# Optimization experiments

Hardware: AMD Instinct MI355X
Metric: run time of the kernel (lower is better)

## Reference

```python
import jax, jax.numpy as jnp
import numpy as np

V, E, H, O = 50000, 256, 256, 2
B, T = 64, 512


def setup_inputs() -> dict:
    key = jax.random.key(0)
    ks = jax.random.split(key, 16)
    s = 0.05
    return {
        "x": jax.random.randint(ks[0], (B, T), 0, V, dtype=jnp.int64),
        "emb": jax.random.normal(ks[1], (V, E), jnp.float32) * s,
        "w_ih_f": jax.random.normal(ks[2], (4 * H, E), jnp.float32) * s,
        "w_hh_f": jax.random.normal(ks[3], (4 * H, H), jnp.float32) * s,
        "b_ih_f": jax.random.normal(ks[4], (4 * H,), jnp.float32) * s,
        "b_hh_f": jax.random.normal(ks[5], (4 * H,), jnp.float32) * s,
        "w_ih_b": jax.random.normal(ks[6], (4 * H, E), jnp.float32) * s,
        "w_hh_b": jax.random.normal(ks[7], (4 * H, H), jnp.float32) * s,
        "b_ih_b": jax.random.normal(ks[8], (4 * H,), jnp.float32) * s,
        "b_hh_b": jax.random.normal(ks[9], (4 * H,), jnp.float32) * s,
        "fc1_w": jax.random.normal(ks[10], (24, 2 * H), jnp.float32) * s,
        "fc1_b": jax.random.normal(ks[11], (24,), jnp.float32) * s,
        "fc2_w": jax.random.normal(ks[12], (O, 24), jnp.float32) * s,
        "fc2_b": jax.random.normal(ks[13], (O,), jnp.float32) * s,
    }


def _run_lstm(xs, Wih, Whh, b):
    # xs: [T, B, E]; PyTorch gate order i, f, g, o
    Bn = xs.shape[1]
    Hn = Whh.shape[1]
    xproj = jnp.einsum('tbe,ge->tbg', xs, Wih) + b  # precompute input projections

    def step(carry, xt):
        h, c = carry
        z = xt + h @ Whh.T
        i, f, g, o = jnp.split(z, 4, axis=-1)
        c = jax.nn.sigmoid(f) * c + jax.nn.sigmoid(i) * jnp.tanh(g)
        h = jax.nn.sigmoid(o) * jnp.tanh(c)
        return (h, c), h

    h0 = jnp.zeros((Bn, Hn), xs.dtype)
    _, ys = jax.lax.scan(step, (h0, h0), xproj)
    return ys  # [T, B, H]


def reference(x, emb, w_ih_f, w_hh_f, b_ih_f, b_hh_f,
              w_ih_b, w_hh_b, b_ih_b, b_hh_b,
              fc1_w, fc1_b, fc2_w, fc2_b):
    embedded = emb[x]                       # [B, T, E]
    xs = jnp.transpose(embedded, (1, 0, 2))  # [T, B, E]
    ys_f = _run_lstm(xs, w_ih_f, w_hh_f, b_ih_f + b_hh_f)          # forward dir
    ys_b = _run_lstm(xs[::-1], w_ih_b, w_hh_b, b_ih_b + b_hh_b)    # backward dir
    # output[:, -1, :] = concat(fwd hidden at t=T-1, bwd hidden at t=T-1)
    # bwd hidden at original t=T-1 is the first step of the reversed scan.
    lstm_out = jnp.concatenate([ys_f[-1], ys_b[0]], axis=-1)  # [B, 2H]
    fc1_out = jax.nn.relu(lstm_out @ fc1_w.T + fc1_b)
    return fc1_out @ fc2_w.T + fc2_b
```

## Files before the change

kernel.cpp:

```cpp
#include <hip/hip_runtime.h>

typedef unsigned int  u32;
typedef unsigned short u16;
typedef unsigned long long u64;
typedef _Float16 half8 __attribute__((ext_vector_type(8)));
typedef short   short8 __attribute__((ext_vector_type(8)));
typedef float   f32x4  __attribute__((ext_vector_type(4)));

#define T_LEN 512
#define BATCH 64
#define EDIM  256
#define HDIM  256
#define G4    1024

static __device__ __forceinline__ u16 f2bf(float f) {
  u32 u = __builtin_bit_cast(u32, f);
  u = (u + 0x7fffu + ((u >> 16) & 1u)) >> 16;
  return (u16)u;
}
static __device__ __forceinline__ u16 f2h(float a) {
  _Float16 ha = (_Float16)a;
  return __builtin_bit_cast(u16, ha);
}
static __device__ __forceinline__ float h2f(u16 a) {
  return (float)__builtin_bit_cast(_Float16, a);
}
static __device__ __forceinline__ float sigf(float x) {
  return __builtin_amdgcn_rcpf(1.0f + __expf(-x));
}
static __device__ __forceinline__ float tanhfast(float x) {
  return fmaf(2.0f, __builtin_amdgcn_rcpf(1.0f + __expf(-2.0f * x)), -1.0f);
}

__global__ __launch_bounds__(256) void k_prep(const float* __restrict__ whh,
                                              u16* __restrict__ Wf,
                                              u16* __restrict__ Wst) {
  int cell = blockIdx.x * 256 + threadIdx.x;
  int mt = cell >> 9, kt = (cell >> 6) & 7, l = cell & 63;
  int gr = mt * 16 + (l & 15);
  int c0 = kt * 32 + (l >> 4) * 8;
  const float4* src = (const float4*)(whh + (size_t)gr * 256 + c0);
  float4 a = src[0], b = src[1];
  u16 o[8] = { f2h(a.x), f2h(a.y), f2h(a.z), f2h(a.w),
               f2h(b.x), f2h(b.y), f2h(b.z), f2h(b.w) };
  *(uint4*)(Wf + (size_t)cell * 8) = *(uint4*)o;
  if (kt >= 6) {
    int q = mt >> 4, jj = mt & 15, s = (kt - 6) * 4 + q;
    *(uint4*)(Wst + ((size_t)(jj * 8 + s) * 64 + l) * 8) = *(uint4*)o;
  }
}

#define LDSPITCH 264
__global__ __launch_bounds__(256) void k_xproj(const int* __restrict__ x,
                                               const float* __restrict__ emb,
                                               const float* __restrict__ wih,
                                               const float* __restrict__ bih,
                                               const float* __restrict__ bhh,
                                               u16* __restrict__ xp2) {
  __shared__ u16 smA[64 * LDSPITCH];
  __shared__ u16 smB[64 * LDSPITCH];
  const int tn = blockIdx.x, t = blockIdx.y;
  const int tid = threadIdx.x;
  const int r = tid >> 2, q4 = tid & 3;

  {
    int eidx = x[r * T_LEN + t];
    const float4* src = (const float4*)(emb + (size_t)eidx * EDIM + q4 * 64);
    u16* dst = smA + r * LDSPITCH + q4 * 64;
    #pragma unroll
    for (int i = 0; i < 16; ++i) {
      float4 v = src[i];
      uint2 p;
      p.x = (u32)f2bf(v.x) | ((u32)f2bf(v.y) << 16);
      p.y = (u32)f2bf(v.z) | ((u32)f2bf(v.w) << 16);
      *(uint2*)&dst[i * 4] = p;
    }
  }
  {
    const float4* src = (const float4*)(wih + (size_t)(tn * 64 + r) * EDIM + q4 * 64);
    u16* dst = smB + r * LDSPITCH + q4 * 64;
    #pragma unroll
    for (int i = 0; i < 16; ++i) {
      float4 v = src[i];
      uint2 p;
      p.x = (u32)f2bf(v.x) | ((u32)f2bf(v.y) << 16);
      p.y = (u32)f2bf(v.z) | ((u32)f2bf(v.w) << 16);
      *(uint2*)&dst[i * 4] = p;
    }
  }
  __syncthreads();

  const int wv = tid >> 6, lane = tid & 63;
  const int lm = lane & 15, q = lane >> 4;
  f32x4 acc[4];
  #pragma unroll
  for (int nt = 0; nt < 4; ++nt) acc[nt] = (f32x4){0.f, 0.f, 0.f, 0.f};

  const u16* pa = smA + (wv * 16 + lm) * LDSPITCH + q * 8;
  const u16* pb = smB + lm * LDSPITCH + q * 8;
  #pragma unroll
  for (int ks = 0; ks < 8; ++ks) {
    short8 av = *(const short8*)(pa + ks * 32);
    #pragma unroll
    for (int nt = 0; nt < 4; ++nt) {
      short8 bv = *(const short8*)(pb + nt * 16 * LDSPITCH + ks * 32);
      acc[nt] = __builtin_amdgcn_mfma_f32_16x16x32_bf16(av, bv, acc[nt], 0, 0, 0);
    }
  }
  #pragma unroll
  for (int nt = 0; nt < 4; ++nt) {
    int g = tn * 64 + nt * 16 + lm;
    float bias = bih[g] + bhh[g];
    int gq = g >> 8, j16 = (g >> 4) & 15, qdd = (g & 15) >> 2, rb = g & 3;
    int mtp = j16 * 4 + gq;
    #pragma unroll
    for (int rr = 0; rr < 4; ++rr) {
      int bl = q * 4 + rr;
      size_t idx = ((((size_t)t * 4 + wv) * 64 + mtp) * 64 + (qdd * 16 + bl)) * 4 + rb;
      xp2[idx] = f2h(acc[nt][rr] + bias);
    }
  }
}

__global__ __launch_bounds__(1024, 4) void k_rnn(const u16* __restrict__ Wf,
                                                 const u16* __restrict__ Wst,
                                                 const u16* __restrict__ xp2,
                                                 u16* __restrict__ hf) {
  extern __shared__ u16 sm[];
  u16* smW = sm;
  u16* smH = sm + 65536;
  const int bg = blockIdx.x;
  const int tid = threadIdx.x;
  const int v = tid >> 6, l = tid & 63;
  const int j = v;
  const int bl = l & 15, qd = l >> 4;

  half8 Wr[4][4];
  #pragma unroll
  for (int q = 0; q < 4; ++q)
    #pragma unroll
    for (int kt = 0; kt < 4; ++kt)
      Wr[q][kt] = *(const half8*)(Wf + ((size_t)((q * 16 + j) * 8 + kt) * 64 + l) * 8);
  #pragma unroll
  for (int q = 0; q < 4; ++q)
    asm volatile("" : "+v"(Wr[q][0]), "+v"(Wr[q][1]), "+v"(Wr[q][2]), "+v"(Wr[q][3]));

  #pragma unroll
  for (int q = 0; q < 4; ++q)
    #pragma unroll
    for (int ki = 0; ki < 2; ++ki) {
      uint4 tv = *(const uint4*)(Wf + ((size_t)((q * 16 + j) * 8 + 4 + ki) * 64 + l) * 8);
      *(uint4*)(smW + ((size_t)(v * 8 + q * 2 + ki) * 512 + l * 8)) = tv;
    }

  {
    u32* hz = (u32*)smH;
    for (int i = tid; i < 4224; i += 1024) hz[i] = 0;
  }
  __syncthreads();

  float c[4] = {0.f, 0.f, 0.f, 0.f};

  const u16* xbase = xp2 + (size_t)bg * 16384 + (size_t)j * 1024 + l * 4;
  const u16* hrd0 = smH + bl * 264 + qd * 8;
  const int  hwof = bl * 264 + j * 16 + qd * 4;
  const u16* wst_l = Wst + (size_t)j * 4096 + l * 8;

  uint2 xA[4], xB[4];
  #pragma unroll
  for (int q = 0; q < 4; ++q)
    xA[q] = *(const uint2*)(xbase + q * 256);

#define STEP(T, XC, XN) do {                                                   \
    u32 zoff = 0;                                                              \
    asm volatile("" : "+v"(zoff));      \
    const u16* wp = wst_l + zoff;                                              \
    uint4 S6[4];                                                               \
    _Pragma("unroll")                                                          \
    for (int q = 0; q < 4; ++q)                                                \
      S6[q] = *(const uint4*)(wp + q * 512);                                   \
    _Pragma("unroll")                             \
    for (int q = 0; q < 4; ++q)                                                \
      XN[q] = *(const uint2*)(xbase + 65536 + q * 256);                        \
    const u16* hb = hrd0 + ((T) & 1) * 4224;                                   \
    f32x4 acc[4];                           \
    _Pragma("unroll")                                                          \
    for (int q = 0; q < 4; ++q)                                                \
      acc[q] = (f32x4){ h2f((u16)XC[q].x), h2f((u16)(XC[q].x >> 16)),          \
                        h2f((u16)XC[q].y), h2f((u16)(XC[q].y >> 16)) };        \
    _Pragma("unroll")                                                          \
    for (int kt = 0; kt < 4; ++kt) {                    \
      half8 Bf = *(const half8*)(hb + kt * 32);                                \
      _Pragma("unroll")                                                        \
      for (int q = 0; q < 4; ++q)                                              \
        acc[q] = __builtin_amdgcn_mfma_f32_16x16x32_f16(Wr[q][kt], Bf,         \
                                                        acc[q], 0, 0, 0);      \
    }                                                                          \
    _Pragma("unroll")                                                          \
    for (int kt = 4; kt < 6; ++kt) {                   \
      half8 Bf = *(const half8*)(hb + kt * 32);                                \
      _Pragma("unroll")                                                        \
      for (int q = 0; q < 4; ++q) {                                            \
        half8 Af = *(const half8*)(smW +                                       \
                     ((size_t)(v * 8 + q * 2 + (kt - 4)) * 512 + l * 8));      \
        acc[q] = __builtin_amdgcn_mfma_f32_16x16x32_f16(Af, Bf,                \
                                                        acc[q], 0, 0, 0);      \
      }                                                                        \
    }                                                                          \
    {                                                                          \
      half8 Bf = *(const half8*)(hb + 6 * 32);        \
      _Pragma("unroll")                                                        \
      for (int q = 0; q < 4; ++q)                                              \
        acc[q] = __builtin_amdgcn_mfma_f32_16x16x32_f16(                       \
            __builtin_bit_cast(half8, S6[q]), Bf, acc[q], 0, 0, 0);            \
    }                                                                          \
    uint4 S7[4];                                             \
    _Pragma("unroll")                                                          \
    for (int q = 0; q < 4; ++q)                                                \
      S7[q] = *(const uint4*)(wp + 2048 + q * 512);                            \
    {                                                                          \
      half8 Bf = *(const half8*)(hb + 7 * 32);                    \
      _Pragma("unroll")                                                        \
      for (int q = 0; q < 4; ++q)                                              \
        acc[q] = __builtin_amdgcn_mfma_f32_16x16x32_f16(                       \
            __builtin_bit_cast(half8, S7[q]), Bf, acc[q], 0, 0, 0);            \
    }                                                                          \
    float hn[4];                         \
    _Pragma("unroll")                                                          \
    for (int r = 0; r < 4; ++r) {                                              \
      float zi = acc[0][r], zf = acc[1][r], zg = acc[2][r], zo = acc[3][r];    \
      c[r] = sigf(zf) * c[r] + sigf(zi) * tanhfast(zg);                        \
      hn[r] = sigf(zo) * tanhfast(c[r]);                                       \
    }                                                                          \
    u32 lo = __builtin_bit_cast(u32, __builtin_amdgcn_cvt_pkrtz(hn[0], hn[1]));\
    u32 hi = __builtin_bit_cast(u32, __builtin_amdgcn_cvt_pkrtz(hn[2], hn[3]));\
    if ((T) == T_LEN - 1) {                                                    \
      *(uint2*)(hf + (size_t)(bg * 16 + bl) * 256 + j * 16 + qd * 4) =         \
          make_uint2(lo, hi);                                                  \
    } else {                                                                   \
      *(uint2*)(smH + (((T) + 1) & 1) * 4224 + hwof) = make_uint2(lo, hi);     \
    }                                                                          \
    xbase += 65536;                                                            \
    asm volatile("s_waitcnt lgkmcnt(0)\n\ts_barrier" ::: "memory");            \
  } while (0)

  for (int tt = 0; tt < T_LEN; tt += 2) {
    STEP(tt, xA, xB);
    STEP(tt + 1, xB, xA);
  }
#undef STEP
}

__global__ __launch_bounds__(256) void k_tail(const int* __restrict__ x,
                                              const float* __restrict__ emb,
                                              const float* __restrict__ wihb,
                                              const float* __restrict__ bihb,
                                              const float* __restrict__ bhhb,
                                              const float* __restrict__ fc1w,
                                              const float* __restrict__ fc1b,
                                              const float* __restrict__ fc2w,
                                              const float* __restrict__ fc2b,
                                              const u16* __restrict__ hf,
                                              float* __restrict__ out) {
  const int b = blockIdx.x, tid = threadIdx.x;
  __shared__ float e[EDIM], hb[HDIM], hfl[HDIM], f1[24];
  e[tid]   = emb[(size_t)x[b * T_LEN + (T_LEN - 1)] * EDIM + tid];
  hfl[tid] = h2f(hf[b * HDIM + tid]);
  __syncthreads();

  float z[4];
  #pragma unroll
  for (int gq = 0; gq < 4; ++gq) {
    int g = gq * HDIM + tid;
    float s = bihb[g] + bhhb[g];
    const float4* wr = (const float4*)(wihb + (size_t)g * EDIM);
    #pragma unroll 8
    for (int k = 0; k < 64; ++k) {
      float4 w = wr[k];
      s += w.x * e[4 * k] + w.y * e[4 * k + 1] + w.z * e[4 * k + 2] + w.w * e[4 * k + 3];
    }
    z[gq] = s;
  }
  float cb = sigf(z[0]) * tanhfast(z[2]);
  hb[tid] = sigf(z[3]) * tanhfast(cb);
  __syncthreads();

  if (tid < 24) {
    float s = fc1b[tid];
    const float* w = fc1w + tid * 512;
    #pragma unroll 8
    for (int k = 0; k < HDIM; ++k) s += w[k] * hfl[k] + w[HDIM + k] * hb[k];
    f1[tid] = fmaxf(s, 0.f);
  }
  __syncthreads();
  if (tid < 2) {
    float s = fc2b[tid];
    #pragma unroll
    for (int k = 0; k < 24; ++k) s += fc2w[tid * 24 + k] * f1[k];
    out[b * 2 + tid] = s;
  }
}

extern "C" void kernel_launch(void* const* d_in, const int* in_sizes, int n_in,
                              void* d_out, int out_size, void* d_ws, size_t ws_size,
                              hipStream_t stream) {
  const int*   x     = (const int*)  d_in[0];
  const float* emb   = (const float*)d_in[1];
  const float* wih_f = (const float*)d_in[2];
  const float* whh_f = (const float*)d_in[3];
  const float* bih_f = (const float*)d_in[4];
  const float* bhh_f = (const float*)d_in[5];
  const float* wih_b = (const float*)d_in[6];
  const float* bih_b = (const float*)d_in[8];
  const float* bhh_b = (const float*)d_in[9];
  const float* fc1w  = (const float*)d_in[10];
  const float* fc1b  = (const float*)d_in[11];
  const float* fc2w  = (const float*)d_in[12];
  const float* fc2b  = (const float*)d_in[13];
  float* out = (float*)d_out;

  char* ws = (char*)d_ws;
  u16* xp2  = (u16*)ws;
  u16* Wf   = (u16*)(ws + 67108864);
  u16* Wst  = (u16*)(ws + 67108864 + 524288);
  u16* hf16 = (u16*)(ws + 67108864 + 524288 + 131072);

  k_prep <<<128, 256, 0, stream>>>(whh_f, Wf, Wst);
  k_xproj<<<dim3(16, 512), 256, 0, stream>>>(x, emb, wih_f, bih_f, bhh_f, xp2);
  k_rnn  <<<4, 1024, 147968, stream>>>(Wf, Wst, xp2, hf16);
  k_tail <<<BATCH, 256, 0, stream>>>(x, emb, wih_b, bih_b, bhh_b,
                                     fc1w, fc1b, fc2w, fc2b, hf16, out);
}
```

Before: 1.491 ms.

## Halve RNN block size, give each wave two hidden slices with more register-resident weights

The recurrent kernel now runs 512 threads per block instead of 1024, and each wave handles two 16-wide hidden slices in sequence. More of the W_hh tiles stay in registers (5 of 8 k-tiles instead of 4), while shared memory and global streaming cover the rest. The intent is cheaper per-step barriers with fewer waves and less weight traffic from LDS and global memory. The cost is twice the serial MFMA work per wave on the critical path and much higher register pressure, which risks spills.

```diff
diff --git a/kernel.cpp b/kernel.cpp
--- a/kernel.cpp
+++ b/kernel.cpp
@@ -122,66 +122,82 @@
   }
 }
 
-__global__ __launch_bounds__(1024, 4) void k_rnn(const u16* __restrict__ Wf,
-                                                 const u16* __restrict__ Wst,
-                                                 const u16* __restrict__ xp2,
-                                                 u16* __restrict__ hf) {
+__global__ __launch_bounds__(512, 2) void k_rnn(const u16* __restrict__ Wf,
+                                                const u16* __restrict__ Wst,
+                                                const u16* __restrict__ xp2,
+                                                u16* __restrict__ hf) {
   extern __shared__ u16 sm[];
   u16* smW = sm;
   u16* smH = sm + 65536;
   const int bg = blockIdx.x;
   const int tid = threadIdx.x;
   const int v = tid >> 6, l = tid & 63;
-  const int j = v;
   const int bl = l & 15, qd = l >> 4;
 
-  half8 Wr[4][4];
-  #pragma unroll
-  for (int q = 0; q < 4; ++q)
-    #pragma unroll
-    for (int kt = 0; kt < 4; ++kt)
-      Wr[q][kt] = *(const half8*)(Wf + ((size_t)((q * 16 + j) * 8 + kt) * 64 + l) * 8);
-  #pragma unroll
-  for (int q = 0; q < 4; ++q)
-    asm volatile("" : "+v"(Wr[q][0]), "+v"(Wr[q][1]), "+v"(Wr[q][2]), "+v"(Wr[q][3]));
-
-  #pragma unroll
-  for (int q = 0; q < 4; ++q)
-    #pragma unroll
-    for (int ki = 0; ki < 2; ++ki) {
-      uint4 tv = *(const uint4*)(Wf + ((size_t)((q * 16 + j) * 8 + 4 + ki) * 64 + l) * 8);
-      *(uint4*)(smW + ((size_t)(v * 8 + q * 2 + ki) * 512 + l * 8)) = tv;
-    }
+  half8 Wr[2][4][5];
+  #pragma unroll
+  for (int p = 0; p < 2; ++p) {
+    const int j = 2 * v + p;
+    #pragma unroll
+    for (int q = 0; q < 4; ++q)
+      #pragma unroll
+      for (int kt = 0; kt < 5; ++kt)
+        Wr[p][q][kt] = *(const half8*)(Wf + ((size_t)((q * 16 + j) * 8 + kt) * 64 + l) * 8);
+  }
+  #pragma unroll
+  for (int p = 0; p < 2; ++p)
+    #pragma unroll
+    for (int q = 0; q < 4; ++q)
+      asm volatile("" : "+v"(Wr[p][q][0]), "+v"(Wr[p][q][1]), "+v"(Wr[p][q][2]),
+                        "+v"(Wr[p][q][3]), "+v"(Wr[p][q][4]));
+
+  #pragma unroll
+  for (int p = 0; p < 2; ++p) {
+    const int j = 2 * v + p;
+    #pragma unroll
+    for (int q = 0; q < 4; ++q)
+      #pragma unroll
+      for (int kt = 5; kt < 7; ++kt) {
+        uint4 tv = *(const uint4*)(Wf + ((size_t)((q * 16 + j) * 8 + kt) * 64 + l) * 8);
+        *(uint4*)(smW + (size_t)(v * 16 + (p * 4 + q) * 2 + (kt - 5)) * 512 + l * 8) = tv;
+      }
+  }
 
   {
     u32* hz = (u32*)smH;
-    for (int i = tid; i < 4224; i += 1024) hz[i] = 0;
-  }
-  __syncthreads();
-
-  float c[4] = {0.f, 0.f, 0.f, 0.f};
-
-  const u16* xbase = xp2 + (size_t)bg * 16384 + (size_t)j * 1024 + l * 4;
+    #pragma unroll
+    for (int k = 0; k < 9; ++k) { int i = tid + k * 512; if (i < 4224) hz[i] = 0; }
+  }
+  __syncthreads();
+
+  float c[2][4];
+  #pragma unroll
+  for (int p = 0; p < 2; ++p)
+    #pragma unroll
+    for (int r = 0; r < 4; ++r) c[p][r] = 0.f;
+
+  const u16* xbase = xp2 + (size_t)bg * 16384 + (size_t)l * 4;
   const u16* hrd0 = smH + bl * 264 + qd * 8;
-  const int  hwof = bl * 264 + j * 16 + qd * 4;
-  const u16* wst_l = Wst + (size_t)j * 4096 + l * 8;
+  const int  hwb  = bl * 264 + qd * 4;
+  const u16* wst0 = Wst + (size_t)(2 * v) * 4096 + l * 8;
 
   uint2 xA[4], xB[4];
   #pragma unroll
   for (int q = 0; q < 4; ++q)
-    xA[q] = *(const uint2*)(xbase + q * 256);
-
-#define STEP(T, XC, XN) do {                                                   \
+    xA[q] = *(const uint2*)(xbase + (size_t)(2 * v) * 1024 + q * 256);
+
+#define PASS(P, XC, XN, NXOFF, T) do {                                         \
+    const int j = 2 * v + (P);                                                 \
     u32 zoff = 0;                                                              \
-    asm volatile("" : "+v"(zoff));      \
-    const u16* wp = wst_l + zoff;                                              \
-    uint4 S6[4];                                                               \
+    asm volatile("" : "+v"(zoff));        \
+    const u16* wp = wst0 + (P) * 4096 + zoff;                                  \
+    uint4 S7[4];                                                               \
     _Pragma("unroll")                                                          \
     for (int q = 0; q < 4; ++q)                                                \
-      S6[q] = *(const uint4*)(wp + q * 512);                                   \
+      S7[q] = *(const uint4*)(wp + (4 + q) * 512);                             \
     _Pragma("unroll")                             \
     for (int q = 0; q < 4; ++q)                                                \
-      XN[q] = *(const uint2*)(xbase + 65536 + q * 256);                        \
+      XN[q] = *(const uint2*)(xbase + (NXOFF) + q * 256);                      \
     const u16* hb = hrd0 + ((T) & 1) * 4224;                                   \
     f32x4 acc[4];                           \
     _Pragma("unroll")                                                          \
@@ -189,37 +205,26 @@
       acc[q] = (f32x4){ h2f((u16)XC[q].x), h2f((u16)(XC[q].x >> 16)),          \
                         h2f((u16)XC[q].y), h2f((u16)(XC[q].y >> 16)) };        \
     _Pragma("unroll")                                                          \
-    for (int kt = 0; kt < 4; ++kt) {                    \
+    for (int kt = 0; kt < 5; ++kt) {                    \
       half8 Bf = *(const half8*)(hb + kt * 32);                                \
       _Pragma("unroll")                                                        \
       for (int q = 0; q < 4; ++q)                                              \
-        acc[q] = __builtin_amdgcn_mfma_f32_16x16x32_f16(Wr[q][kt], Bf,         \
+        acc[q] = __builtin_amdgcn_mfma_f32_16x16x32_f16(Wr[P][q][kt], Bf,      \
                                                         acc[q], 0, 0, 0);      \
     }                                                                          \
     _Pragma("unroll")                                                          \
-    for (int kt = 4; kt < 6; ++kt) {                   \
+    for (int kt = 5; kt < 7; ++kt) {                   \
       half8 Bf = *(const half8*)(hb + kt * 32);                                \
       _Pragma("unroll")                                                        \
       for (int q = 0; q < 4; ++q) {                                            \
         half8 Af = *(const half8*)(smW +                                       \
-                     ((size_t)(v * 8 + q * 2 + (kt - 4)) * 512 + l * 8));      \
+            (size_t)(v * 16 + ((P) * 4 + q) * 2 + (kt - 5)) * 512 + l * 8);    \
         acc[q] = __builtin_amdgcn_mfma_f32_16x16x32_f16(Af, Bf,                \
                                                         acc[q], 0, 0, 0);      \
       }                                                                        \
     }                                                                          \
     {                                                                          \
-      half8 Bf = *(const half8*)(hb + 6 * 32);        \
-      _Pragma("unroll")                                                        \
-      for (int q = 0; q < 4; ++q)                                              \
-        acc[q] = __builtin_amdgcn_mfma_f32_16x16x32_f16(                       \
-            __builtin_bit_cast(half8, S6[q]), Bf, acc[q], 0, 0, 0);            \
-    }                                                                          \
-    uint4 S7[4];                                             \
-    _Pragma("unroll")                                                          \
-    for (int q = 0; q < 4; ++q)                                                \
-      S7[q] = *(const uint4*)(wp + 2048 + q * 512);                            \
-    {                                                                          \
-      half8 Bf = *(const half8*)(hb + 7 * 32);                    \
+      half8 Bf = *(const half8*)(hb + 7 * 32);           \
       _Pragma("unroll")                                                        \
       for (int q = 0; q < 4; ++q)                                              \
         acc[q] = __builtin_amdgcn_mfma_f32_16x16x32_f16(                       \
@@ -229,8 +234,8 @@
     _Pragma("unroll")                                                          \
     for (int r = 0; r < 4; ++r) {                                              \
       float zi = acc[0][r], zf = acc[1][r], zg = acc[2][r], zo = acc[3][r];    \
-      c[r] = sigf(zf) * c[r] + sigf(zi) * tanhfast(zg);                        \
-      hn[r] = sigf(zo) * tanhfast(c[r]);                                       \
+      c[P][r] = sigf(zf) * c[P][r] + sigf(zi) * tanhfast(zg);                  \
+      hn[r] = sigf(zo) * tanhfast(c[P][r]);                                    \
     }                                                                          \
     u32 lo = __builtin_bit_cast(u32, __builtin_amdgcn_cvt_pkrtz(hn[0], hn[1]));\
     u32 hi = __builtin_bit_cast(u32, __builtin_amdgcn_cvt_pkrtz(hn[2], hn[3]));\
@@ -238,17 +243,18 @@
       *(uint2*)(hf + (size_t)(bg * 16 + bl) * 256 + j * 16 + qd * 4) =         \
           make_uint2(lo, hi);                                                  \
     } else {                                                                   \
-      *(uint2*)(smH + (((T) + 1) & 1) * 4224 + hwof) = make_uint2(lo, hi);     \
-    }                                                                          \
-    xbase += 65536;                                                            \
-    asm volatile("s_waitcnt lgkmcnt(0)\n\ts_barrier" ::: "memory");            \
+      *(uint2*)(smH + (((T) + 1) & 1) * 4224 + hwb + j * 16) =                 \
+          make_uint2(lo, hi);                                                  \
+    }                                                                          \
   } while (0)
 
-  for (int tt = 0; tt < T_LEN; tt += 2) {
-    STEP(tt, xA, xB);
-    STEP(tt + 1, xB, xA);
-  }
-#undef STEP
+  for (int t = 0; t < T_LEN; ++t) {
+    PASS(0, xA, xB, (size_t)(2 * v + 1) * 1024, t);
+    PASS(1, xB, xA, 65536 + (size_t)(2 * v) * 1024, t);
+    xbase += 65536;
+    asm volatile("s_waitcnt lgkmcnt(0)\n\ts_barrier" ::: "memory");
+  }
+#undef PASS
 }
 
 __global__ __launch_bounds__(256) void k_tail(const int* __restrict__ x,
@@ -327,7 +333,7 @@
 
   k_prep <<<128, 256, 0, stream>>>(whh_f, Wf, Wst);
   k_xproj<<<dim3(16, 512), 256, 0, stream>>>(x, emb, wih_f, bih_f, bhh_f, xp2);
-  k_rnn  <<<4, 1024, 147968, stream>>>(Wf, Wst, xp2, hf16);
+  k_rnn  <<<4, 512, 147968, stream>>>(Wf, Wst, xp2, hf16);
   k_tail <<<BATCH, 256, 0, stream>>>(x, emb, wih_b, bih_b, bhh_b,
                                      fc1w, fc1b, fc2w, fc2b, hf16, out);
 }
```

New measurement: 1.588 ms. 6.5% more time.
